# Kernel optimization log

Hardware: AMD Instinct MI355X
Metric: run time of the kernel (lower is better)

## Reference

```python
import jax, jax.numpy as jnp
import numpy as np

T, B, I, H, L = 512, 4096, 23, 20, 2  # seq len, batch, input dim, hidden dim, num layers


def setup_inputs() -> dict:
    key = jax.random.key(0)
    ks = jax.random.split(key, 13)
    s = 1.0 / np.sqrt(H)  # pytorch default uniform bound scale (use normal*s for simplicity)
    f32 = jnp.float32
    return {
        "x": jax.random.normal(ks[0], (T, B, I), f32),
        "h0": jax.random.normal(ks[1], (L, B, H), f32),
        "c0": jax.random.normal(ks[2], (L, B, H), f32),
        "W_ih0": jax.random.normal(ks[3], (4 * H, I), f32) * s,
        "W_hh0": jax.random.normal(ks[4], (4 * H, H), f32) * s,
        "b_ih0": jax.random.normal(ks[5], (4 * H,), f32) * s,
        "b_hh0": jax.random.normal(ks[6], (4 * H,), f32) * s,
        "W_ih1": jax.random.normal(ks[7], (4 * H, H), f32) * s,
        "W_hh1": jax.random.normal(ks[8], (4 * H, H), f32) * s,
        "b_ih1": jax.random.normal(ks[9], (4 * H,), f32) * s,
        "b_hh1": jax.random.normal(ks[10], (4 * H,), f32) * s,
        "W_lin": jax.random.normal(ks[11], (1, H), f32) * s,
        "b_lin": jax.random.normal(ks[12], (1,), f32) * s,
    }


def _lstm_layer(xs, h0, c0, W_ih, W_hh, b_ih, b_hh):
    # Precompute input contributions for all timesteps at once: [T, B, 4H]
    xg = jnp.einsum('tbi,gi->tbg', xs, W_ih) + b_ih + b_hh

    def step(carry, xg_t):
        h, c = carry
        gates = xg_t + h @ W_hh.T          # [B, 4H]
        i, f, g, o = jnp.split(gates, 4, axis=-1)  # pytorch gate order: i, f, g, o
        c = jax.nn.sigmoid(f) * c + jax.nn.sigmoid(i) * jnp.tanh(g)
        h = jax.nn.sigmoid(o) * jnp.tanh(c)
        return (h, c), h

    _, hs = jax.lax.scan(step, (h0, c0), xg)
    return hs  # [T, B, H]


def reference(x, h0, c0, W_ih0, W_hh0, b_ih0, b_hh0, W_ih1, W_hh1, b_ih1, b_hh1, W_lin, b_lin):
    out = _lstm_layer(x, h0[0], c0[0], W_ih0, W_hh0, b_ih0, b_hh0)
    out = _lstm_layer(out, h0[1], c0[1], W_ih1, W_hh1, b_ih1, b_hh1)
    y = jax.nn.relu(out)                   # relu(lstm output), [T, B, H]
    # lin applied then time-index 6 selected; equivalent (and cheaper) to index first
    z6 = y[6] @ W_lin.T + b_lin            # [B, 1]
    return jax.nn.relu(z6)
```

## Files before the change

kernel.cpp:

```cpp
#include <hip/hip_runtime.h>
#include <math.h>


constexpr int kT  = 7;
constexpr int kI  = 23;
constexpr int kH  = 20;
constexpr int kG  = 80;
constexpr int kBT = 16;
constexpr int kThreads = 320;

__device__ __forceinline__ float sigm(float v) {
    return 1.0f / (1.0f + __expf(-v));
}
__device__ __forceinline__ float tanh_(float v) {
    float e = __expf(2.0f * v);
    return 1.0f - 2.0f / (e + 1.0f);
}

__global__ __launch_bounds__(kThreads) void lstm7_kernel(
    const float* __restrict__ x,
    const float* __restrict__ h0,
    const float* __restrict__ c0,
    const float* __restrict__ Wih0,
    const float* __restrict__ Whh0,
    const float* __restrict__ bih0,
    const float* __restrict__ bhh0,
    const float* __restrict__ Wih1,
    const float* __restrict__ Whh1,
    const float* __restrict__ bih1,
    const float* __restrict__ bhh1,
    const float* __restrict__ Wlin,
    const float* __restrict__ blin,
    float* __restrict__ out,
    int B)
{
    __shared__ __align__(16) float xT[kT][kI][kH];
    __shared__ __align__(16) float gT[kG][kH];
    __shared__ __align__(16) float h1T[kH][kH];
    __shared__ __align__(16) float h2T[kH][kH];

    const int tid = threadIdx.x;
    const int b0  = blockIdx.x * kBT;

    for (int idx = tid; idx < kT * kBT * kI; idx += kThreads) {
        int t = idx / (kBT * kI);
        int r = idx % (kBT * kI);
        int b = r / kI;
        int i = r % kI;
        xT[t][i][b] = x[((size_t)t * B + (b0 + b)) * kI + i];
    }

    const int g  = tid % kG;
    const int bq = tid / kG;

    float wA[kI], wB[kH], wC[kH], wD[kH];
#pragma unroll
    for (int k = 0; k < kI; ++k) wA[k] = Wih0[g * kI + k];
#pragma unroll
    for (int k = 0; k < kH; ++k) wB[k] = Whh0[g * kH + k];
#pragma unroll
    for (int k = 0; k < kH; ++k) wC[k] = Wih1[g * kH + k];
#pragma unroll
    for (int k = 0; k < kH; ++k) wD[k] = Whh1[g * kH + k];
    const float bias1 = bih0[g] + bhh0[g];
    const float bias2 = bih1[g] + bhh1[g];

    const int pb = tid / kH;
    const int pu = tid % kH;
    float c1 = c0[(size_t)0 * B * kH + (size_t)(b0 + pb) * kH + pu];
    float c2 = c0[(size_t)1 * B * kH + (size_t)(b0 + pb) * kH + pu];
    h1T[pu][pb] = h0[(size_t)0 * B * kH + (size_t)(b0 + pb) * kH + pu];
    h2T[pu][pb] = h0[(size_t)1 * B * kH + (size_t)(b0 + pb) * kH + pu];

    __syncthreads();

    for (int t = 0; t < kT; ++t) {
        float a0 = bias1, a1 = bias1, a2 = bias1, a3 = bias1;
#pragma unroll
        for (int k = 0; k < kI; ++k) {
            const float4 v = *reinterpret_cast<const float4*>(&xT[t][k][bq * 4]);
            a0 = fmaf(wA[k], v.x, a0);
            a1 = fmaf(wA[k], v.y, a1);
            a2 = fmaf(wA[k], v.z, a2);
            a3 = fmaf(wA[k], v.w, a3);
        }
#pragma unroll
        for (int k = 0; k < kH; ++k) {
            const float4 v = *reinterpret_cast<const float4*>(&h1T[k][bq * 4]);
            a0 = fmaf(wB[k], v.x, a0);
            a1 = fmaf(wB[k], v.y, a1);
            a2 = fmaf(wB[k], v.z, a2);
            a3 = fmaf(wB[k], v.w, a3);
        }
        *reinterpret_cast<float4*>(&gT[g][bq * 4]) = make_float4(a0, a1, a2, a3);
        __syncthreads();

        {
            const float gi = gT[pu][pb];
            const float gf = gT[kH + pu][pb];
            const float gc = gT[2 * kH + pu][pb];
            const float go = gT[3 * kH + pu][pb];
            c1 = sigm(gf) * c1 + sigm(gi) * tanh_(gc);
            h1T[pu][pb] = sigm(go) * tanh_(c1);
        }
        __syncthreads();

        a0 = bias2; a1 = bias2; a2 = bias2; a3 = bias2;
#pragma unroll
        for (int k = 0; k < kH; ++k) {
            const float4 v = *reinterpret_cast<const float4*>(&h1T[k][bq * 4]);
            a0 = fmaf(wC[k], v.x, a0);
            a1 = fmaf(wC[k], v.y, a1);
            a2 = fmaf(wC[k], v.z, a2);
            a3 = fmaf(wC[k], v.w, a3);
        }
#pragma unroll
        for (int k = 0; k < kH; ++k) {
            const float4 v = *reinterpret_cast<const float4*>(&h2T[k][bq * 4]);
            a0 = fmaf(wD[k], v.x, a0);
            a1 = fmaf(wD[k], v.y, a1);
            a2 = fmaf(wD[k], v.z, a2);
            a3 = fmaf(wD[k], v.w, a3);
        }
        *reinterpret_cast<float4*>(&gT[g][bq * 4]) = make_float4(a0, a1, a2, a3);
        __syncthreads();

        {
            const float gi = gT[pu][pb];
            const float gf = gT[kH + pu][pb];
            const float gc = gT[2 * kH + pu][pb];
            const float go = gT[3 * kH + pu][pb];
            c2 = sigm(gf) * c2 + sigm(gi) * tanh_(gc);
            h2T[pu][pb] = sigm(go) * tanh_(c2);
        }
        __syncthreads();
    }

    if (tid < kBT) {
        const int b = tid;
        float acc = blin[0];
#pragma unroll
        for (int u = 0; u < kH; ++u) {
            acc = fmaf(fmaxf(h2T[u][b], 0.0f), Wlin[u], acc);
        }
        out[b0 + b] = fmaxf(acc, 0.0f);
    }
}

extern "C" void kernel_launch(void* const* d_in, const int* in_sizes, int n_in,
                              void* d_out, int out_size, void* d_ws, size_t ws_size,
                              hipStream_t stream) {
    const float* x    = (const float*)d_in[0];
    const float* h0   = (const float*)d_in[1];
    const float* c0   = (const float*)d_in[2];
    const float* Wih0 = (const float*)d_in[3];
    const float* Whh0 = (const float*)d_in[4];
    const float* bih0 = (const float*)d_in[5];
    const float* bhh0 = (const float*)d_in[6];
    const float* Wih1 = (const float*)d_in[7];
    const float* Whh1 = (const float*)d_in[8];
    const float* bih1 = (const float*)d_in[9];
    const float* bhh1 = (const float*)d_in[10];
    const float* Wlin = (const float*)d_in[11];
    const float* blin = (const float*)d_in[12];
    float* out = (float*)d_out;

    const int B = in_sizes[1] / (2 * kH);
    const int blocks = B / kBT;

    hipLaunchKernelGGL(lstm7_kernel, dim3(blocks), dim3(kThreads), 0, stream,
                       x, h0, c0, Wih0, Whh0, bih0, bhh0,
                       Wih1, Whh1, bih1, bhh1, Wlin, blin, out, B);
}
```

Before: 23.66 us.

## Exchange LSTM gates via DPP quad broadcast and double-buffer hidden state

Threads are regrouped so the four gates of one hidden unit sit in adjacent lanes of a quad. DPP quad-permute moves gate values between those lanes, which removes the shared-memory gate buffer and two of the four barriers per timestep. Hidden state is double-buffered, the batch tile drops from 16 to 8 so there are twice as many blocks, and launch bounds ask for 3 blocks per CU. Activations use raw exp2/rcp intrinsics, and split accumulators shorten the FMA dependency chains. Each lane now computes the redundant cell update for all four gates, and the smaller tile doubles how often weights are loaded per block.

```diff
diff --git a/kernel.cpp b/kernel.cpp
--- a/kernel.cpp
+++ b/kernel.cpp
@@ -6,18 +6,29 @@
 constexpr int kI  = 23;
 constexpr int kH  = 20;
 constexpr int kG  = 80;
-constexpr int kBT = 16;
+constexpr int kBT = 8;
 constexpr int kThreads = 320;
 
 __device__ __forceinline__ float sigm(float v) {
-    return 1.0f / (1.0f + __expf(-v));
+    return __builtin_amdgcn_rcpf(1.0f + __builtin_amdgcn_exp2f(v * -1.44269504f));
 }
 __device__ __forceinline__ float tanh_(float v) {
-    float e = __expf(2.0f * v);
-    return 1.0f - 2.0f / (e + 1.0f);
+    return 1.0f - 2.0f * __builtin_amdgcn_rcpf(__builtin_amdgcn_exp2f(v * 2.88539008f) + 1.0f);
+}
+template<int J>
+__device__ __forceinline__ float qb(float v) {
+    return __int_as_float(__builtin_amdgcn_mov_dpp(__float_as_int(v), J * 0x55, 0xF, 0xF, true));
+}
+__device__ __forceinline__ void lstm_update(float a, float& c, float& h) {
+    const float gi = qb<0>(a);
+    const float gf = qb<1>(a);
+    const float gg = qb<2>(a);
+    const float go = qb<3>(a);
+    c = sigm(gf) * c + sigm(gi) * tanh_(gg);
+    h = sigm(go) * tanh_(c);
 }
 
-__global__ __launch_bounds__(kThreads) void lstm7_kernel(
+__global__ __launch_bounds__(kThreads, 3) void lstm7_kernel(
     const float* __restrict__ x,
     const float* __restrict__ h0,
     const float* __restrict__ c0,
@@ -34,104 +45,105 @@
     float* __restrict__ out,
     int B)
 {
-    __shared__ __align__(16) float xT[kT][kI][kH];
-    __shared__ __align__(16) float gT[kG][kH];
-    __shared__ __align__(16) float h1T[kH][kH];
-    __shared__ __align__(16) float h2T[kH][kH];
+    __shared__ __align__(16) float xS[kT][kI][kBT];
+    __shared__ __align__(16) float h1S[2][kH][kBT];
+    __shared__ __align__(16) float h2S[2][kH][kBT];
 
     const int tid = threadIdx.x;
     const int b0  = blockIdx.x * kBT;
+    const int bp  = tid / kG;
+    const int q   = tid & 3;
+    const int u   = (tid % kG) >> 2;
+    const int grow = q * kH + u;
+    const int bb  = bp * 2;
 
-    for (int idx = tid; idx < kT * kBT * kI; idx += kThreads) {
-        int t = idx / (kBT * kI);
-        int r = idx % (kBT * kI);
-        int b = r / kI;
-        int i = r % kI;
-        xT[t][i][b] = x[((size_t)t * B + (b0 + b)) * kI + i];
+    for (int idx = tid; idx < kT * kI * kBT; idx += kThreads) {
+        const int t = idx / (kI * kBT);
+        const int r = idx % (kI * kBT);
+        const int i = r / kBT;
+        const int b = r % kBT;
+        xS[t][i][b] = x[((size_t)t * B + b0 + b) * kI + i];
+    }
+    if (tid < kH * kBT) {
+        const int uu = tid / kBT, b = tid % kBT;
+        h1S[0][uu][b] = h0[(size_t)(b0 + b) * kH + uu];
+        h2S[0][uu][b] = h0[(size_t)(B + b0 + b) * kH + uu];
     }
 
-    const int g  = tid % kG;
-    const int bq = tid / kG;
+    float wA[kI], wB[kH], wC[kH], wD[kH];
+    {
+        const float* pa = Wih0 + grow * kI;
+#pragma unroll
+        for (int k = 0; k < kI; ++k) wA[k] = pa[k];
+        const float4* pb = reinterpret_cast<const float4*>(Whh0 + grow * kH);
+        const float4* pc = reinterpret_cast<const float4*>(Wih1 + grow * kH);
+        const float4* pd = reinterpret_cast<const float4*>(Whh1 + grow * kH);
+#pragma unroll
+        for (int j = 0; j < 5; ++j) {
+            const float4 vb = pb[j], vc = pc[j], vd = pd[j];
+            wB[4*j] = vb.x; wB[4*j+1] = vb.y; wB[4*j+2] = vb.z; wB[4*j+3] = vb.w;
+            wC[4*j] = vc.x; wC[4*j+1] = vc.y; wC[4*j+2] = vc.z; wC[4*j+3] = vc.w;
+            wD[4*j] = vd.x; wD[4*j+1] = vd.y; wD[4*j+2] = vd.z; wD[4*j+3] = vd.w;
+        }
+    }
+    const float bias1 = bih0[grow] + bhh0[grow];
+    const float bias2 = bih1[grow] + bhh1[grow];
 
-    float wA[kI], wB[kH], wC[kH], wD[kH];
-#pragma unroll
-    for (int k = 0; k < kI; ++k) wA[k] = Wih0[g * kI + k];
-#pragma unroll
-    for (int k = 0; k < kH; ++k) wB[k] = Whh0[g * kH + k];
-#pragma unroll
-    for (int k = 0; k < kH; ++k) wC[k] = Wih1[g * kH + k];
-#pragma unroll
-    for (int k = 0; k < kH; ++k) wD[k] = Whh1[g * kH + k];
-    const float bias1 = bih0[g] + bhh0[g];
-    const float bias2 = bih1[g] + bhh1[g];
-
-    const int pb = tid / kH;
-    const int pu = tid % kH;
-    float c1 = c0[(size_t)0 * B * kH + (size_t)(b0 + pb) * kH + pu];
-    float c2 = c0[(size_t)1 * B * kH + (size_t)(b0 + pb) * kH + pu];
-    h1T[pu][pb] = h0[(size_t)0 * B * kH + (size_t)(b0 + pb) * kH + pu];
-    h2T[pu][pb] = h0[(size_t)1 * B * kH + (size_t)(b0 + pb) * kH + pu];
+    float2 c1, c2;
+    c1.x = c0[(size_t)(b0 + bb) * kH + u];
+    c1.y = c0[(size_t)(b0 + bb + 1) * kH + u];
+    c2.x = c0[(size_t)(B + b0 + bb) * kH + u];
+    c2.y = c0[(size_t)(B + b0 + bb + 1) * kH + u];
 
     __syncthreads();
 
+#pragma unroll
     for (int t = 0; t < kT; ++t) {
-        float a0 = bias1, a1 = bias1, a2 = bias1, a3 = bias1;
+        const int rb = t & 1, wb = rb ^ 1;
+
+        float a0 = bias1, a1 = bias1, e0 = 0.f, e1 = 0.f;
 #pragma unroll
         for (int k = 0; k < kI; ++k) {
-            const float4 v = *reinterpret_cast<const float4*>(&xT[t][k][bq * 4]);
-            a0 = fmaf(wA[k], v.x, a0);
-            a1 = fmaf(wA[k], v.y, a1);
-            a2 = fmaf(wA[k], v.z, a2);
-            a3 = fmaf(wA[k], v.w, a3);
+            const float2 v = *reinterpret_cast<const float2*>(&xS[t][k][bb]);
+            if (k & 1) { e0 = fmaf(wA[k], v.x, e0); e1 = fmaf(wA[k], v.y, e1); }
+            else       { a0 = fmaf(wA[k], v.x, a0); a1 = fmaf(wA[k], v.y, a1); }
         }
 #pragma unroll
         for (int k = 0; k < kH; ++k) {
-            const float4 v = *reinterpret_cast<const float4*>(&h1T[k][bq * 4]);
-            a0 = fmaf(wB[k], v.x, a0);
-            a1 = fmaf(wB[k], v.y, a1);
-            a2 = fmaf(wB[k], v.z, a2);
-            a3 = fmaf(wB[k], v.w, a3);
+            const float2 v = *reinterpret_cast<const float2*>(&h1S[rb][k][bb]);
+            if (k & 1) { e0 = fmaf(wB[k], v.x, e0); e1 = fmaf(wB[k], v.y, e1); }
+            else       { a0 = fmaf(wB[k], v.x, a0); a1 = fmaf(wB[k], v.y, a1); }
         }
-        *reinterpret_cast<float4*>(&gT[g][bq * 4]) = make_float4(a0, a1, a2, a3);
-        __syncthreads();
+        a0 += e0; a1 += e1;
 
         {
-            const float gi = gT[pu][pb];
-            const float gf = gT[kH + pu][pb];
-            const float gc = gT[2 * kH + pu][pb];
-            const float go = gT[3 * kH + pu][pb];
-            c1 = sigm(gf) * c1 + sigm(gi) * tanh_(gc);
-            h1T[pu][pb] = sigm(go) * tanh_(c1);
+            float hx, hy;
+            lstm_update(a0, c1.x, hx);
+            lstm_update(a1, c1.y, hy);
+            if (q == 0) *reinterpret_cast<float2*>(&h1S[wb][u][bb]) = make_float2(hx, hy);
         }
         __syncthreads();
 
-        a0 = bias2; a1 = bias2; a2 = bias2; a3 = bias2;
+        float g0 = bias2, g1 = bias2, f0 = 0.f, f1 = 0.f;
 #pragma unroll
         for (int k = 0; k < kH; ++k) {
-            const float4 v = *reinterpret_cast<const float4*>(&h1T[k][bq * 4]);
-            a0 = fmaf(wC[k], v.x, a0);
-            a1 = fmaf(wC[k], v.y, a1);
-            a2 = fmaf(wC[k], v.z, a2);
-            a3 = fmaf(wC[k], v.w, a3);
+            const float2 v = *reinterpret_cast<const float2*>(&h1S[wb][k][bb]);
+            if (k & 1) { f0 = fmaf(wC[k], v.x, f0); f1 = fmaf(wC[k], v.y, f1); }
+            else       { g0 = fmaf(wC[k], v.x, g0); g1 = fmaf(wC[k], v.y, g1); }
         }
 #pragma unroll
         for (int k = 0; k < kH; ++k) {
-            const float4 v = *reinterpret_cast<const float4*>(&h2T[k][bq * 4]);
-            a0 = fmaf(wD[k], v.x, a0);
-            a1 = fmaf(wD[k], v.y, a1);
-            a2 = fmaf(wD[k], v.z, a2);
-            a3 = fmaf(wD[k], v.w, a3);
+            const float2 v = *reinterpret_cast<const float2*>(&h2S[rb][k][bb]);
+            if (k & 1) { f0 = fmaf(wD[k], v.x, f0); f1 = fmaf(wD[k], v.y, f1); }
+            else       { g0 = fmaf(wD[k], v.x, g0); g1 = fmaf(wD[k], v.y, g1); }
         }
-        *reinterpret_cast<float4*>(&gT[g][bq * 4]) = make_float4(a0, a1, a2, a3);
-        __syncthreads();
+        g0 += f0; g1 += f1;
 
         {
-            const float gi = gT[pu][pb];
-            const float gf = gT[kH + pu][pb];
-            const float gc = gT[2 * kH + pu][pb];
-            const float go = gT[3 * kH + pu][pb];
-            c2 = sigm(gf) * c2 + sigm(gi) * tanh_(gc);
-            h2T[pu][pb] = sigm(go) * tanh_(c2);
+            float hx, hy;
+            lstm_update(g0, c2.x, hx);
+            lstm_update(g1, c2.y, hy);
+            if (q == 0) *reinterpret_cast<float2*>(&h2S[wb][u][bb]) = make_float2(hx, hy);
         }
         __syncthreads();
     }
@@ -140,8 +152,8 @@
         const int b = tid;
         float acc = blin[0];
 #pragma unroll
-        for (int u = 0; u < kH; ++u) {
-            acc = fmaf(fmaxf(h2T[u][b], 0.0f), Wlin[u], acc);
+        for (int uu = 0; uu < kH; ++uu) {
+            acc = fmaf(fmaxf(h2S[1][uu][b], 0.0f), Wlin[uu], acc);
         }
         out[b0 + b] = fmaxf(acc, 0.0f);
     }
```

Result: slower. 24.93 us (+5.4%).
